# Kernel optimization log

Measured on AMD Instinct MI355X. Metric: run time of the kernel, lower is better.

Reference implementation:

```python
import math
import jax, jax.numpy as jnp
import numpy as np

D_MODEL = 1024
D_STATE = 64
BATCH = 8
SEQLEN = 2048


def setup_inputs() -> dict:
    key = jax.random.key(0)
    ks = jax.random.split(key, 8)
    x = jax.random.normal(ks[0], (BATCH, SEQLEN, D_MODEL), dtype=jnp.float32)
    # faithful init: lam_real = -0.5 -> log_Lam_real = log(0.5); Lam_imag = pi*arange(N)
    log_Lam_real = jnp.log(0.5 * jnp.ones((D_STATE,), dtype=jnp.float32))
    Lam_imag = math.pi * jnp.arange(D_STATE, dtype=jnp.float32)
    B_real = 0.02 * jax.random.normal(ks[1], (D_STATE, D_MODEL), dtype=jnp.float32)
    B_imag = 0.02 * jax.random.normal(ks[2], (D_STATE, D_MODEL), dtype=jnp.float32)
    C_real = 0.02 * jax.random.normal(ks[3], (D_MODEL, D_STATE), dtype=jnp.float32)
    C_imag = 0.02 * jax.random.normal(ks[4], (D_MODEL, D_STATE), dtype=jnp.float32)
    Dp = jnp.ones((D_MODEL,), dtype=jnp.float32)
    log_dt = jnp.zeros((1,), dtype=jnp.float32)
    W_out = 0.02 * jax.random.normal(ks[5], (D_MODEL, D_MODEL), dtype=jnp.float32)
    b_out = jnp.zeros((D_MODEL,), dtype=jnp.float32)
    return {"x": x, "log_Lam_real": log_Lam_real, "Lam_imag": Lam_imag,
            "B_real": B_real, "B_imag": B_imag, "C_real": C_real, "C_imag": C_imag,
            "D": Dp, "log_dt": log_dt, "W_out": W_out, "b_out": b_out}


def reference(x, log_Lam_real, Lam_imag, B_real, B_imag, C_real, C_imag, D, log_dt, W_out, b_out):
    B, L, H = x.shape
    N = log_Lam_real.shape[0]
    dt = jnp.exp(log_dt)                          # (1,)
    Lam_r = -jnp.exp(log_Lam_real)                # (N,)
    mag = jnp.exp(Lam_r * dt)                     # (N,)
    Lbar_r = mag * jnp.cos(Lam_imag * dt)         # (N,)
    Lbar_i = mag * jnp.sin(Lam_imag * dt)         # (N,)
    # batched input projection for all timesteps: (B,L,N)
    Bu_r = jnp.einsum('blh,nh->bln', x, dt * B_real)
    Bu_i = jnp.einsum('blh,nh->bln', x, dt * B_imag)

    def step(carry, bu):
        sr, si = carry
        bur, bui = bu
        nr = Lbar_r * sr - Lbar_i * si + bur
        ni = Lbar_r * si + Lbar_i * sr + bui
        return (nr, ni), (nr, ni)

    sr0 = jnp.zeros((B, N), dtype=x.dtype)
    si0 = jnp.zeros((B, N), dtype=x.dtype)
    (sr, si), (SR, SI) = jax.lax.scan(
        step, (sr0, si0),
        (jnp.swapaxes(Bu_r, 0, 1), jnp.swapaxes(Bu_i, 0, 1)))  # scan over L; SR,SI: (L,B,N)
    # output: y_t = Re(C x_t) + D*u_t, vectorized over all t
    y = jnp.einsum('lbn,hn->blh', SR, C_real) - jnp.einsum('lbn,hn->blh', SI, C_imag) + D * x
    out = y @ W_out.T + b_out                     # out_proj (dropout is identity, p=0)
    return out, (sr, si)
```

## Files before the change

kernel.cpp:

```cpp
#include <hip/hip_runtime.h>

#define HD 1024
#define NS 64
#define NB 8
#define LS 2048
#define MT (NB*LS)
#define N2 128
#define KA 1152
#define CHL 16
#define NCH (LS/CHL)

typedef __attribute__((ext_vector_type(8))) short short8;
typedef __attribute__((ext_vector_type(4))) float f32x4;

#define OB_ABUF 0u
#define OB_BMAT (OB_ABUF + MT*KA*2)
#define OB_BMP  (OB_BMAT + HD*KA*2)
#define OB_BU   (OB_BMP  + N2*HD*2)
#define OB_FR   (OB_BU   + MT*N2*4)
#define OB_FI   (OB_FR   + NB*NS*NCH*4)
#define OB_CR   (OB_FI   + NB*NS*NCH*4)
#define OB_CI   (OB_CR   + NB*NS*NCH*4)
#define OB_WB   (OB_CI   + NB*NS*NCH*4)
#define OB_CCT  (OB_WB   + HD*HD*2)

__device__ __forceinline__ unsigned short f2bf(float f) {
    unsigned u = __float_as_uint(f);
    u = (u + 0x7FFFu + ((u >> 16) & 1u)) >> 16;
    return (unsigned short)u;
}

__device__ __forceinline__ void lbar_of(int n, const float* __restrict__ logLr,
                                        const float* __restrict__ Li, float dt,
                                        float& ar, float& ai) {
    float lr  = -expf(logLr[n]);
    float mag = expf(lr * dt);
    float ang = Li[n] * dt;
    ar = mag * cosf(ang);
    ai = mag * sinf(ang);
}

__global__ __launch_bounds__(256) void k_prep(const float* __restrict__ x,
                                              const float* __restrict__ W,
                                              const float* __restrict__ Dv,
                                              const float* __restrict__ Br,
                                              const float* __restrict__ Bi,
                                              const float* __restrict__ log_dt,
                                              unsigned short* __restrict__ Ab,
                                              unsigned short* __restrict__ Bm,
                                              unsigned short* __restrict__ Bp,
                                              unsigned short* __restrict__ Wb) {
    const int blk = blockIdx.x;
    if (blk < 8192) {
        size_t idx = ((size_t)blk * 256 + threadIdx.x) * 8;
        int m = (int)(idx >> 10), k = (int)(idx & 1023);
        float4 v0 = *(const float4*)&x[idx];
        float4 v1 = *(const float4*)&x[idx + 4];
        short8 s;
        s[0]=f2bf(v0.x); s[1]=f2bf(v0.y); s[2]=f2bf(v0.z); s[3]=f2bf(v0.w);
        s[4]=f2bf(v1.x); s[5]=f2bf(v1.y); s[6]=f2bf(v1.z); s[7]=f2bf(v1.w);
        *(short8*)&Ab[(size_t)m * KA + k] = s;
    } else if (blk < 8704) {
        size_t idx = ((size_t)(blk - 8192) * 256 + threadIdx.x) * 8;
        int h = (int)(idx >> 10), k = (int)(idx & 1023);
        float4 v0 = *(const float4*)&W[idx];
        float4 v1 = *(const float4*)&W[idx + 4];
        float4 d0 = *(const float4*)&Dv[k];
        float4 d1 = *(const float4*)&Dv[k + 4];
        short8 s;
        s[0]=f2bf(v0.x*d0.x); s[1]=f2bf(v0.y*d0.y); s[2]=f2bf(v0.z*d0.z); s[3]=f2bf(v0.w*d0.w);
        s[4]=f2bf(v1.x*d1.x); s[5]=f2bf(v1.y*d1.y); s[6]=f2bf(v1.z*d1.z); s[7]=f2bf(v1.w*d1.w);
        *(short8*)&Bm[(size_t)h * KA + k] = s;
    } else if (blk < 8768) {
        size_t idx = ((size_t)(blk - 8704) * 256 + threadIdx.x) * 8;
        int n2 = (int)(idx >> 10), k = (int)(idx & 1023);
        float dt = expf(log_dt[0]);
        const float* src = (n2 < NS) ? &Br[(size_t)n2 * HD + k] : &Bi[(size_t)(n2 - NS) * HD + k];
        float4 v0 = *(const float4*)&src[0];
        float4 v1 = *(const float4*)&src[4];
        short8 s;
        s[0]=f2bf(v0.x*dt); s[1]=f2bf(v0.y*dt); s[2]=f2bf(v0.z*dt); s[3]=f2bf(v0.w*dt);
        s[4]=f2bf(v1.x*dt); s[5]=f2bf(v1.y*dt); s[6]=f2bf(v1.z*dt); s[7]=f2bf(v1.w*dt);
        *(short8*)&Bp[(size_t)n2 * HD + k] = s;
    } else {
        size_t idx = ((size_t)(blk - 8768) * 256 + threadIdx.x) * 8;
        float4 v0 = *(const float4*)&W[idx];
        float4 v1 = *(const float4*)&W[idx + 4];
        short8 s;
        s[0]=f2bf(v0.x); s[1]=f2bf(v0.y); s[2]=f2bf(v0.z); s[3]=f2bf(v0.w);
        s[4]=f2bf(v1.x); s[5]=f2bf(v1.y); s[6]=f2bf(v1.z); s[7]=f2bf(v1.w);
        *(short8*)&Wb[idx] = s;
    }
}

__global__ __launch_bounds__(256) void k_tcc(const float* __restrict__ Cr,
                                             const float* __restrict__ Ci,
                                             unsigned short* __restrict__ CCT) {
    __shared__ float T[64][65];
    const int h0 = blockIdx.x * 64;
    const int half = blockIdx.y;
    const float* src = half ? Ci : Cr;
    const float sgn = half ? -1.f : 1.f;
    const int tid = threadIdx.x;
    const int j = tid & 63, i4 = tid >> 6;
    #pragma unroll
    for (int p = 0; p < 16; ++p) {
        int i = p * 4 + i4;
        T[i][j] = src[(size_t)(h0 + i) * NS + j];
    }
    __syncthreads();
    #pragma unroll
    for (int p = 0; p < 16; ++p) {
        int jj = p * 4 + i4;
        CCT[(size_t)(half * NS + jj) * HD + h0 + j] = f2bf(sgn * T[j][jj]);
    }
}

__global__ __launch_bounds__(256) void k_carry(const float* __restrict__ Bu,
                                               const float* __restrict__ logLr,
                                               const float* __restrict__ Li,
                                               const float* __restrict__ log_dt,
                                               float* __restrict__ Fr,
                                               float* __restrict__ Fi) {
    int g = blockIdx.x * 256 + threadIdx.x;
    int n = g & 63, ch = (g >> 6) & (NCH - 1), b = g >> 13;
    float dt = expf(log_dt[0]);
    float ar, ai; lbar_of(n, logLr, Li, dt, ar, ai);
    float sr = 0.f, si = 0.f;
    size_t base = ((size_t)b * LS + ch * CHL) * N2;
    #pragma unroll 4
    for (int j = 0; j < CHL; ++j) {
        float ur = Bu[base + j * N2 + n];
        float ui = Bu[base + j * N2 + NS + n];
        float nr = ar * sr - ai * si + ur;
        float ni = ar * si + ai * sr + ui;
        sr = nr; si = ni;
    }
    int fi = (b * NS + n) * NCH + ch;
    Fr[fi] = sr; Fi[fi] = si;
}

__global__ __launch_bounds__(256) void k_scan2(const float* __restrict__ Fr,
                                               const float* __restrict__ Fi,
                                               const float* __restrict__ logLr,
                                               const float* __restrict__ Li,
                                               const float* __restrict__ log_dt,
                                               float* __restrict__ CexR,
                                               float* __restrict__ CexI,
                                               float* __restrict__ out_tail) {
    int g = blockIdx.x * 256 + threadIdx.x;
    if (g >= NB * NS) return;
    int n = g & 63;
    float dt = expf(log_dt[0]);
    float ar, ai; lbar_of(n, logLr, Li, dt, ar, ai);
    float Ar = ar, Ai = ai;
    #pragma unroll
    for (int s = 0; s < 4; ++s) { float nr = Ar*Ar - Ai*Ai; Ai = 2.f*Ar*Ai; Ar = nr; }
    float cr = 0.f, ci = 0.f;
    for (int ch = 0; ch < NCH; ++ch) {
        CexR[g * NCH + ch] = cr; CexI[g * NCH + ch] = ci;
        float fr = Fr[g * NCH + ch], fi2 = Fi[g * NCH + ch];
        float nr = Ar * cr - Ai * ci + fr;
        float ni = Ar * ci + Ai * cr + fi2;
        cr = nr; ci = ni;
    }
    out_tail[g]          = cr;
    out_tail[NB*NS + g]  = ci;
}

__global__ __launch_bounds__(256) void k_scan3(const float* __restrict__ Bu,
                                               const float* __restrict__ CexR,
                                               const float* __restrict__ CexI,
                                               const float* __restrict__ logLr,
                                               const float* __restrict__ Li,
                                               const float* __restrict__ log_dt,
                                               unsigned short* __restrict__ Ab) {
    int g = blockIdx.x * 256 + threadIdx.x;
    int n = g & 63, ch = (g >> 6) & (NCH - 1), b = g >> 13;
    float dt = expf(log_dt[0]);
    float ar, ai; lbar_of(n, logLr, Li, dt, ar, ai);
    int ci_idx = (b * NS + n) * NCH + ch;
    float sr = CexR[ci_idx], si = CexI[ci_idx];
    size_t base = ((size_t)b * LS + ch * CHL);
    #pragma unroll 4
    for (int j = 0; j < CHL; ++j) {
        size_t m = base + j;
        float ur = Bu[m * N2 + n];
        float ui = Bu[m * N2 + NS + n];
        float nr = ar * sr - ai * si + ur;
        float ni = ar * si + ai * sr + ui;
        sr = nr; si = ni;
        Ab[m * KA + HD + n]      = f2bf(sr);
        Ab[m * KA + HD + NS + n] = f2bf(si);
    }
}

template<int KTOT, int LDB, int LDO, bool BIAS, bool BF16OUT>
__global__ __launch_bounds__(256) void k_mfma_gemm(const unsigned short* __restrict__ A,
                                                   int lda,
                                                   const unsigned short* __restrict__ B,
                                                   const float* __restrict__ bias,
                                                   void* __restrict__ outp) {
    __shared__ unsigned short At[128 * 32];
    __shared__ unsigned short Bt[128 * 32];
    const int m0 = blockIdx.x * 128, n0 = blockIdx.y * 128;
    const int tid = threadIdx.x, wv = tid >> 6, ln = tid & 63;
    const int wr = wv >> 1, wc = wv & 1;
    const int r16 = ln & 15, kg = ln >> 4;
    f32x4 zero = {0.f, 0.f, 0.f, 0.f};
    f32x4 acc[4][4];
    #pragma unroll
    for (int i = 0; i < 4; ++i)
        #pragma unroll
        for (int j = 0; j < 4; ++j) acc[i][j] = zero;

    for (int kt = 0; kt < KTOT; kt += 32) {
        #pragma unroll
        for (int i = 0; i < 2; ++i) {
            int e = i * 4096 + wv * 1024 + ln * 16;
            int row = e >> 6, kb = e & 63;
            const char* ga = (const char*)A + ((size_t)(m0 + row) * lda + kt) * 2 + kb;
            __builtin_amdgcn_global_load_lds(
                (const __attribute__((address_space(1))) void*)ga,
                (__attribute__((address_space(3))) void*)((char*)At + i * 4096 + wv * 1024),
                16, 0, 0);
            const char* gb = (const char*)B + ((size_t)(n0 + row) * LDB + kt) * 2 + kb;
            __builtin_amdgcn_global_load_lds(
                (const __attribute__((address_space(1))) void*)gb,
                (__attribute__((address_space(3))) void*)((char*)Bt + i * 4096 + wv * 1024),
                16, 0, 0);
        }
        __syncthreads();
        short8 af[4], bfr[4];
        #pragma unroll
        for (int i = 0; i < 4; ++i) {
            af[i]  = *(const short8*)&At[(wr * 64 + i * 16 + r16) * 32 + kg * 8];
            bfr[i] = *(const short8*)&Bt[(wc * 64 + i * 16 + r16) * 32 + kg * 8];
        }
        #pragma unroll
        for (int i = 0; i < 4; ++i)
            #pragma unroll
            for (int j = 0; j < 4; ++j)
                acc[i][j] = __builtin_amdgcn_mfma_f32_16x16x32_bf16(af[i], bfr[j], acc[i][j], 0, 0, 0);
        __syncthreads();
    }
    #pragma unroll
    for (int j = 0; j < 4; ++j) {
        int col = n0 + wc * 64 + j * 16 + r16;
        float bv = BIAS ? bias[col] : 0.f;
        #pragma unroll
        for (int i = 0; i < 4; ++i) {
            #pragma unroll
            for (int r = 0; r < 4; ++r) {
                int row = m0 + wr * 64 + i * 16 + kg * 4 + r;
                if (BF16OUT) ((unsigned short*)outp)[(size_t)row * LDO + col] = f2bf(acc[i][j][r] + bv);
                else         ((float*)outp)[(size_t)row * LDO + col] = acc[i][j][r] + bv;
            }
        }
    }
}

extern "C" void kernel_launch(void* const* d_in, const int* in_sizes, int n_in,
                              void* d_out, int out_size, void* d_ws, size_t ws_size,
                              hipStream_t stream) {
    const float* x      = (const float*)d_in[0];
    const float* logLr  = (const float*)d_in[1];
    const float* Li     = (const float*)d_in[2];
    const float* Br     = (const float*)d_in[3];
    const float* Bi     = (const float*)d_in[4];
    const float* Cr     = (const float*)d_in[5];
    const float* Ci     = (const float*)d_in[6];
    const float* Dv     = (const float*)d_in[7];
    const float* log_dt = (const float*)d_in[8];
    const float* W      = (const float*)d_in[9];
    const float* bo     = (const float*)d_in[10];
    float* out = (float*)d_out;
    char*  ws  = (char*)d_ws;

    unsigned short* Abuf = (unsigned short*)(ws + OB_ABUF);
    unsigned short* Bmat = (unsigned short*)(ws + OB_BMAT);
    unsigned short* Bmp  = (unsigned short*)(ws + OB_BMP);
    float* Bu   = (float*)(ws + OB_BU);
    float* Fr   = (float*)(ws + OB_FR);
    float* Fi   = (float*)(ws + OB_FI);
    float* CexR = (float*)(ws + OB_CR);
    float* CexI = (float*)(ws + OB_CI);
    unsigned short* Wb   = (unsigned short*)(ws + OB_WB);
    unsigned short* CCT  = (unsigned short*)(ws + OB_CCT);

    k_prep <<<9280, 256, 0, stream>>>(x, W, Dv, Br, Bi, log_dt, Abuf, Bmat, Bmp, Wb);
    k_tcc  <<<dim3(16, 2), 256, 0, stream>>>(Cr, Ci, CCT);
    k_mfma_gemm<1024, 1024, KA, false, true><<<dim3(HD / 128, 1), 256, 0, stream>>>(
        Wb, HD, CCT, nullptr, Bmat + HD);
    k_mfma_gemm<1024, 1024, 128, false, false><<<dim3(MT / 128, 1), 256, 0, stream>>>(
        Abuf, KA, Bmp, nullptr, Bu);
    k_carry<<<(NB * NS * NCH) / 256, 256, 0, stream>>>(Bu, logLr, Li, log_dt, Fr, Fi);
    k_scan2<<<2, 256, 0, stream>>>(Fr, Fi, logLr, Li, log_dt, CexR, CexI, out + (size_t)MT * HD);
    k_scan3<<<(NB * NS * NCH) / 256, 256, 0, stream>>>(Bu, CexR, CexI, logLr, Li, log_dt, Abuf);
    k_mfma_gemm<KA, KA, HD, true, false><<<dim3(MT / 128, HD / 128), 256, 0, stream>>>(
        Abuf, KA, Bmat, bo, out);
}
```

Baseline: 263.8 us.

## Triple-buffer GEMM loads, merge small launches, transpose scan carry layout

The MFMA GEMM body gets a three-stage LDS ring buffer filled by async global_load_lds. Explicit vmcnt waits and barriers let the loads for tile t+3 overlap the MFMAs on tile t, and s_setprio raises priority during the MFMA block. The C transpose kernel is folded into k_prep, and the two small GEMMs (input projection and W·C fold) are merged into one launch, cutting launch count and filling more CUs. The chunk-carry arrays are relaid out chunk-major so that k_scan2's sequential loop reads and writes coalesced across threads. In exchange, the ring buffer triples LDS per block, which may reduce occupancy, and the GEMM loses compile-time template parameters.

```diff
diff --git a/kernel.cpp b/kernel.cpp
--- a/kernel.cpp
+++ b/kernel.cpp
@@ -9,6 +9,7 @@
 #define KA 1152
 #define CHL 16
 #define NCH (LS/CHL)
+#define NG  (NB*NS)
 
 typedef __attribute__((ext_vector_type(8))) short short8;
 typedef __attribute__((ext_vector_type(4))) float f32x4;
@@ -18,10 +19,10 @@
 #define OB_BMP  (OB_BMAT + HD*KA*2)
 #define OB_BU   (OB_BMP  + N2*HD*2)
 #define OB_FR   (OB_BU   + MT*N2*4)
-#define OB_FI   (OB_FR   + NB*NS*NCH*4)
-#define OB_CR   (OB_FI   + NB*NS*NCH*4)
-#define OB_CI   (OB_CR   + NB*NS*NCH*4)
-#define OB_WB   (OB_CI   + NB*NS*NCH*4)
+#define OB_FI   (OB_FR   + NG*NCH*4)
+#define OB_CR   (OB_FI   + NG*NCH*4)
+#define OB_CI   (OB_CR   + NG*NCH*4)
+#define OB_WB   (OB_CI   + NG*NCH*4)
 #define OB_CCT  (OB_WB   + HD*HD*2)
 
 __device__ __forceinline__ unsigned short f2bf(float f) {
@@ -45,11 +46,15 @@
                                               const float* __restrict__ Dv,
                                               const float* __restrict__ Br,
                                               const float* __restrict__ Bi,
+                                              const float* __restrict__ Cr,
+                                              const float* __restrict__ Ci,
                                               const float* __restrict__ log_dt,
                                               unsigned short* __restrict__ Ab,
                                               unsigned short* __restrict__ Bm,
                                               unsigned short* __restrict__ Bp,
-                                              unsigned short* __restrict__ Wb) {
+                                              unsigned short* __restrict__ Wb,
+                                              unsigned short* __restrict__ CCT) {
+    __shared__ float T[64][65];
     const int blk = blockIdx.x;
     if (blk < 8192) {
         size_t idx = ((size_t)blk * 256 + threadIdx.x) * 8;
@@ -82,7 +87,7 @@
         s[0]=f2bf(v0.x*dt); s[1]=f2bf(v0.y*dt); s[2]=f2bf(v0.z*dt); s[3]=f2bf(v0.w*dt);
         s[4]=f2bf(v1.x*dt); s[5]=f2bf(v1.y*dt); s[6]=f2bf(v1.z*dt); s[7]=f2bf(v1.w*dt);
         *(short8*)&Bp[(size_t)n2 * HD + k] = s;
-    } else {
+    } else if (blk < 9280) {
         size_t idx = ((size_t)(blk - 8768) * 256 + threadIdx.x) * 8;
         float4 v0 = *(const float4*)&W[idx];
         float4 v1 = *(const float4*)&W[idx + 4];
@@ -90,29 +95,25 @@
         s[0]=f2bf(v0.x); s[1]=f2bf(v0.y); s[2]=f2bf(v0.z); s[3]=f2bf(v0.w);
         s[4]=f2bf(v1.x); s[5]=f2bf(v1.y); s[6]=f2bf(v1.z); s[7]=f2bf(v1.w);
         *(short8*)&Wb[idx] = s;
-    }
-}
-
-__global__ __launch_bounds__(256) void k_tcc(const float* __restrict__ Cr,
-                                             const float* __restrict__ Ci,
-                                             unsigned short* __restrict__ CCT) {
-    __shared__ float T[64][65];
-    const int h0 = blockIdx.x * 64;
-    const int half = blockIdx.y;
-    const float* src = half ? Ci : Cr;
-    const float sgn = half ? -1.f : 1.f;
-    const int tid = threadIdx.x;
-    const int j = tid & 63, i4 = tid >> 6;
-    #pragma unroll
-    for (int p = 0; p < 16; ++p) {
-        int i = p * 4 + i4;
-        T[i][j] = src[(size_t)(h0 + i) * NS + j];
-    }
-    __syncthreads();
-    #pragma unroll
-    for (int p = 0; p < 16; ++p) {
-        int jj = p * 4 + i4;
-        CCT[(size_t)(half * NS + jj) * HD + h0 + j] = f2bf(sgn * T[j][jj]);
+    } else {
+        const int local = blk - 9280;
+        const int h0 = (local & 15) * 64;
+        const int half = local >> 4;
+        const float* src = half ? Ci : Cr;
+        const float sgn = half ? -1.f : 1.f;
+        const int tid = threadIdx.x;
+        const int j = tid & 63, i4 = tid >> 6;
+        #pragma unroll
+        for (int p = 0; p < 16; ++p) {
+            int i = p * 4 + i4;
+            T[i][j] = src[(size_t)(h0 + i) * NS + j];
+        }
+        __syncthreads();
+        #pragma unroll
+        for (int p = 0; p < 16; ++p) {
+            int jj = p * 4 + i4;
+            CCT[(size_t)(half * NS + jj) * HD + h0 + j] = f2bf(sgn * T[j][jj]);
+        }
     }
 }
 
@@ -136,7 +137,7 @@
         float ni = ar * si + ai * sr + ui;
         sr = nr; si = ni;
     }
-    int fi = (b * NS + n) * NCH + ch;
+    int fi = ch * NG + b * 64 + n;
     Fr[fi] = sr; Fi[fi] = si;
 }
 
@@ -149,7 +150,7 @@
                                                float* __restrict__ CexI,
                                                float* __restrict__ out_tail) {
     int g = blockIdx.x * 256 + threadIdx.x;
-    if (g >= NB * NS) return;
+    if (g >= NG) return;
     int n = g & 63;
     float dt = expf(log_dt[0]);
     float ar, ai; lbar_of(n, logLr, Li, dt, ar, ai);
@@ -158,14 +159,14 @@
     for (int s = 0; s < 4; ++s) { float nr = Ar*Ar - Ai*Ai; Ai = 2.f*Ar*Ai; Ar = nr; }
     float cr = 0.f, ci = 0.f;
     for (int ch = 0; ch < NCH; ++ch) {
-        CexR[g * NCH + ch] = cr; CexI[g * NCH + ch] = ci;
-        float fr = Fr[g * NCH + ch], fi2 = Fi[g * NCH + ch];
+        CexR[ch * NG + g] = cr; CexI[ch * NG + g] = ci;
+        float fr = Fr[ch * NG + g], fi2 = Fi[ch * NG + g];
         float nr = Ar * cr - Ai * ci + fr;
         float ni = Ar * ci + Ai * cr + fi2;
         cr = nr; ci = ni;
     }
-    out_tail[g]          = cr;
-    out_tail[NB*NS + g]  = ci;
+    out_tail[g]       = cr;
+    out_tail[NG + g]  = ci;
 }
 
 __global__ __launch_bounds__(256) void k_scan3(const float* __restrict__ Bu,
@@ -179,7 +180,7 @@
     int n = g & 63, ch = (g >> 6) & (NCH - 1), b = g >> 13;
     float dt = expf(log_dt[0]);
     float ar, ai; lbar_of(n, logLr, Li, dt, ar, ai);
-    int ci_idx = (b * NS + n) * NCH + ch;
+    int ci_idx = ch * NG + b * 64 + n;
     float sr = CexR[ci_idx], si = CexI[ci_idx];
     size_t base = ((size_t)b * LS + ch * CHL);
     #pragma unroll 4
@@ -195,15 +196,15 @@
     }
 }
 
-template<int KTOT, int LDB, int LDO, bool BIAS, bool BF16OUT>
-__global__ __launch_bounds__(256) void k_mfma_gemm(const unsigned short* __restrict__ A,
-                                                   int lda,
-                                                   const unsigned short* __restrict__ B,
-                                                   const float* __restrict__ bias,
-                                                   void* __restrict__ outp) {
-    __shared__ unsigned short At[128 * 32];
-    __shared__ unsigned short Bt[128 * 32];
-    const int m0 = blockIdx.x * 128, n0 = blockIdx.y * 128;
+template<int KTOT>
+__device__ __forceinline__ void gemm_body(const unsigned short* __restrict__ A, int lda,
+                                          const unsigned short* __restrict__ B, int ldb,
+                                          const float* __restrict__ bias, int has_bias,
+                                          void* __restrict__ outp, int ldo, int bf16out,
+                                          int m0, int n0) {
+    constexpr int T = KTOT / 32;
+    __shared__ unsigned short At[3][128 * 32];
+    __shared__ unsigned short Bt[3][128 * 32];
     const int tid = threadIdx.x, wv = tid >> 6, ln = tid & 63;
     const int wr = wv >> 1, wc = wv & 1;
     const int r16 = ln & 15, kg = ln >> 4;
@@ -214,7 +215,8 @@
         #pragma unroll
         for (int j = 0; j < 4; ++j) acc[i][j] = zero;
 
-    for (int kt = 0; kt < KTOT; kt += 32) {
+    auto STAGE = [&](int t, int s) {
+        const int kt = t * 32;
         #pragma unroll
         for (int i = 0; i < 2; ++i) {
             int e = i * 4096 + wv * 1024 + ln * 16;
@@ -222,41 +224,76 @@
             const char* ga = (const char*)A + ((size_t)(m0 + row) * lda + kt) * 2 + kb;
             __builtin_amdgcn_global_load_lds(
                 (const __attribute__((address_space(1))) void*)ga,
-                (__attribute__((address_space(3))) void*)((char*)At + i * 4096 + wv * 1024),
+                (__attribute__((address_space(3))) void*)((char*)At[s] + i * 4096 + wv * 1024),
                 16, 0, 0);
-            const char* gb = (const char*)B + ((size_t)(n0 + row) * LDB + kt) * 2 + kb;
+            const char* gb = (const char*)B + ((size_t)(n0 + row) * ldb + kt) * 2 + kb;
             __builtin_amdgcn_global_load_lds(
                 (const __attribute__((address_space(1))) void*)gb,
-                (__attribute__((address_space(3))) void*)((char*)Bt + i * 4096 + wv * 1024),
+                (__attribute__((address_space(3))) void*)((char*)Bt[s] + i * 4096 + wv * 1024),
                 16, 0, 0);
         }
-        __syncthreads();
+    };
+
+    STAGE(0, 0); STAGE(1, 1); STAGE(2, 2);
+    int s = 0;
+    for (int t = 0; t < T; ++t) {
+        if (t + 2 < T)      asm volatile("s_waitcnt vmcnt(8)" ::: "memory");
+        else if (t + 1 < T) asm volatile("s_waitcnt vmcnt(4)" ::: "memory");
+        else                asm volatile("s_waitcnt vmcnt(0)" ::: "memory");
+        __builtin_amdgcn_s_barrier();
+        asm volatile("" ::: "memory");
         short8 af[4], bfr[4];
         #pragma unroll
         for (int i = 0; i < 4; ++i) {
-            af[i]  = *(const short8*)&At[(wr * 64 + i * 16 + r16) * 32 + kg * 8];
-            bfr[i] = *(const short8*)&Bt[(wc * 64 + i * 16 + r16) * 32 + kg * 8];
-        }
+            af[i]  = *(const short8*)&At[s][(wr * 64 + i * 16 + r16) * 32 + kg * 8];
+            bfr[i] = *(const short8*)&Bt[s][(wc * 64 + i * 16 + r16) * 32 + kg * 8];
+        }
+        __builtin_amdgcn_s_setprio(1);
         #pragma unroll
         for (int i = 0; i < 4; ++i)
             #pragma unroll
             for (int j = 0; j < 4; ++j)
                 acc[i][j] = __builtin_amdgcn_mfma_f32_16x16x32_bf16(af[i], bfr[j], acc[i][j], 0, 0, 0);
-        __syncthreads();
+        __builtin_amdgcn_s_setprio(0);
+        asm volatile("" ::: "memory");
+        __builtin_amdgcn_s_barrier();
+        if (t + 3 < T) STAGE(t + 3, s);
+        if (++s == 3) s = 0;
     }
     #pragma unroll
     for (int j = 0; j < 4; ++j) {
         int col = n0 + wc * 64 + j * 16 + r16;
-        float bv = BIAS ? bias[col] : 0.f;
+        float bv = has_bias ? bias[col] : 0.f;
         #pragma unroll
         for (int i = 0; i < 4; ++i) {
             #pragma unroll
             for (int r = 0; r < 4; ++r) {
                 int row = m0 + wr * 64 + i * 16 + kg * 4 + r;
-                if (BF16OUT) ((unsigned short*)outp)[(size_t)row * LDO + col] = f2bf(acc[i][j][r] + bv);
-                else         ((float*)outp)[(size_t)row * LDO + col] = acc[i][j][r] + bv;
+                if (bf16out) ((unsigned short*)outp)[(size_t)row * ldo + col] = f2bf(acc[i][j][r] + bv);
+                else         ((float*)outp)[(size_t)row * ldo + col] = acc[i][j][r] + bv;
             }
         }
+    }
+}
+
+__global__ __launch_bounds__(256) void k_gemm_big(const unsigned short* __restrict__ A,
+                                                  const unsigned short* __restrict__ B,
+                                                  const float* __restrict__ bias,
+                                                  float* __restrict__ out) {
+    gemm_body<KA>(A, KA, B, KA, bias, 1, out, HD, 0, blockIdx.x * 128, blockIdx.y * 128);
+}
+
+__global__ __launch_bounds__(256) void k_gemm_small(const unsigned short* __restrict__ Abuf,
+                                                    const unsigned short* __restrict__ Bmp,
+                                                    const unsigned short* __restrict__ Wb,
+                                                    const unsigned short* __restrict__ CCT,
+                                                    float* __restrict__ Bu,
+                                                    unsigned short* __restrict__ BmE2) {
+    const int bx = blockIdx.x;
+    if (bx < 128) {
+        gemm_body<1024>(Abuf, KA, Bmp, 1024, nullptr, 0, Bu, 128, 0, bx * 128, 0);
+    } else {
+        gemm_body<1024>(Wb, 1024, CCT, 1024, nullptr, 0, BmE2, KA, 1, (bx - 128) * 128, 0);
     }
 }
 
@@ -288,15 +325,10 @@
     unsigned short* Wb   = (unsigned short*)(ws + OB_WB);
     unsigned short* CCT  = (unsigned short*)(ws + OB_CCT);
 
-    k_prep <<<9280, 256, 0, stream>>>(x, W, Dv, Br, Bi, log_dt, Abuf, Bmat, Bmp, Wb);
-    k_tcc  <<<dim3(16, 2), 256, 0, stream>>>(Cr, Ci, CCT);
-    k_mfma_gemm<1024, 1024, KA, false, true><<<dim3(HD / 128, 1), 256, 0, stream>>>(
-        Wb, HD, CCT, nullptr, Bmat + HD);
-    k_mfma_gemm<1024, 1024, 128, false, false><<<dim3(MT / 128, 1), 256, 0, stream>>>(
-        Abuf, KA, Bmp, nullptr, Bu);
+    k_prep <<<9312, 256, 0, stream>>>(x, W, Dv, Br, Bi, Cr, Ci, log_dt, Abuf, Bmat, Bmp, Wb, CCT);
+    k_gemm_small<<<136, 256, 0, stream>>>(Abuf, Bmp, Wb, CCT, Bu, Bmat + HD);
     k_carry<<<(NB * NS * NCH) / 256, 256, 0, stream>>>(Bu, logLr, Li, log_dt, Fr, Fi);
     k_scan2<<<2, 256, 0, stream>>>(Fr, Fi, logLr, Li, log_dt, CexR, CexI, out + (size_t)MT * HD);
     k_scan3<<<(NB * NS * NCH) / 256, 256, 0, stream>>>(Bu, CexR, CexI, logLr, Li, log_dt, Abuf);
-    k_mfma_gemm<KA, KA, HD, true, false><<<dim3(MT / 128, HD / 128), 256, 0, stream>>>(
-        Abuf, KA, Bmat, bo, out);
-}
+    k_gemm_big<<<dim3(MT / 128, HD / 128), 256, 0, stream>>>(Abuf, Bmat, bo, out);
+}
```

New measurement: 234.0 us. 1.13x faster.
